# Optimization experiments

Measured on AMD Instinct MI355X. Metric: run time of the kernel, lower is better.

Reference implementation:

```python
import jax, jax.numpy as jnp
import numpy as np

D = 2048
HQ = 32
HKV = 8
DH = D // HQ          # 64
GROUP = HQ // HKV     # 4
B, T = 2, 2048


def setup_inputs() -> dict:
    key = jax.random.key(0)
    ks = jax.random.split(key, 5)
    s = 0.02
    return {
        "x": jax.random.normal(ks[0], (B, T, D), dtype=jnp.float32),
        "Wq": jax.random.normal(ks[1], (D, D), dtype=jnp.float32) * s,
        "Wk": jax.random.normal(ks[2], (D, HKV * DH), dtype=jnp.float32) * s,
        "Wv": jax.random.normal(ks[3], (D, HKV * DH), dtype=jnp.float32) * s,
        "Wo": jax.random.normal(ks[4], (D, D), dtype=jnp.float32) * s,
    }


def reference(x, Wq, Wk, Wv, Wo):
    Bsz, Tlen, _ = x.shape
    # projections
    q = (x @ Wq).reshape(Bsz, Tlen, HQ, DH).transpose(0, 2, 1, 3)    # [B,hq,T,dh]
    k = (x @ Wk).reshape(Bsz, Tlen, HKV, DH).transpose(0, 2, 1, 3)   # [B,hkv,T,dh]
    v = (x @ Wv).reshape(Bsz, Tlen, HKV, DH).transpose(0, 2, 1, 3)
    # GQA: repeat each kv head GROUP times along the head dim
    k = jnp.repeat(k, GROUP, axis=1)                                  # [B,hq,T,dh]
    v = jnp.repeat(v, GROUP, axis=1)
    scale = 1.0 / jnp.sqrt(jnp.asarray(DH, dtype=x.dtype))
    att = jnp.einsum("bhqd,bhkd->bhqk", q, k) * scale                # [B,hq,T,T]
    p = jax.nn.softmax(att, axis=-1)
    out = jnp.einsum("bhqk,bhkd->bhqd", p, v)                        # [B,hq,T,dh]
    out = out.transpose(0, 2, 1, 3).reshape(Bsz, Tlen, D)            # [B,T,D]
    return out @ Wo
```

## Files before the change

kernel.cpp:

```cpp
#include <hip/hip_runtime.h>
#include <stdint.h>

typedef __bf16 bf16;
typedef __bf16 bf16x8 __attribute__((ext_vector_type(8)));
typedef __bf16 bf16x4_t __attribute__((ext_vector_type(4)));
typedef __bf16 bf16x2_t __attribute__((ext_vector_type(2)));
typedef float f32x4 __attribute__((ext_vector_type(4)));
typedef float f32x16 __attribute__((ext_vector_type(16)));
typedef unsigned int u32x4 __attribute__((ext_vector_type(4)));

#define HQ_N 32
#define DH_N 64
#define SEQ 2048
#define NTOK 4096

#if __has_builtin(__builtin_amdgcn_exp2f)
#define EXP2(x) __builtin_amdgcn_exp2f(x)
#else
#define EXP2(x) __expf((x) * 0.69314718056f)
#endif

#define QSCALE 0.18033688011112042f

__device__ __forceinline__ void async_ld16(const bf16* g, bf16* l) {
    __builtin_amdgcn_global_load_lds(
        (__attribute__((address_space(1))) void*)(uintptr_t)(g),
        (__attribute__((address_space(3))) void*)(uint32_t)(uintptr_t)(l),
        16, 0, 0);
}

__device__ __forceinline__ void perm32swap(unsigned &x, unsigned &y) {
#if __has_builtin(__builtin_amdgcn_permlane32_swap)
    auto r = __builtin_amdgcn_permlane32_swap((int)x, (int)y, false, false);
    x = (unsigned)r[0]; y = (unsigned)r[1];
#else
    asm("v_permlane32_swap_b32 %0, %1" : "+v"(x), "+v"(y));
#endif
}

__global__ __launch_bounds__(256) void k_prep(
    const float* __restrict__ x,
    const float* __restrict__ Wq, const float* __restrict__ Wk,
    const float* __restrict__ Wv, const float* __restrict__ Wo,
    bf16* __restrict__ xb, bf16* __restrict__ WqkvT, bf16* __restrict__ WoT)
{
    const int z = blockIdx.z;
    const int tid = threadIdx.x;

    if (z >= 4) {
        int i = ((z - 4) * 1024 + blockIdx.y * 32 + blockIdx.x) * 256 + tid;
        float4 f = ((const float4*)x)[i];
        bf16x4_t v = {(bf16)f.x, (bf16)f.y, (bf16)f.z, (bf16)f.w};
        ((bf16x4_t*)xb)[i] = v;
        return;
    }

    const float* in; bf16* out; int C;
    const int R = 2048;
    if      (z == 0) { in = Wq; out = WqkvT;                        C = 2048; }
    else if (z == 1) { in = Wk; out = WqkvT + (size_t)2048 * 2048;  C = 512;  }
    else if (z == 2) { in = Wv; out = WqkvT + (size_t)2560 * 2048;  C = 512;  }
    else             { in = Wo; out = WoT;                          C = 2048; }
    if (blockIdx.x * 64 >= C) return;

    __shared__ float t[64][65];
    const int c0 = blockIdx.x * 64, r0 = blockIdx.y * 64;
#pragma unroll
    for (int c = 0; c < 4; ++c) {
        int i = tid + c * 256;
        int row = i >> 4, cc = (i & 15) * 4;
        float4 v = *(const float4*)(in + (size_t)(r0 + row) * C + c0 + cc);
        t[row][cc + 0] = v.x; t[row][cc + 1] = v.y;
        t[row][cc + 2] = v.z; t[row][cc + 3] = v.w;
    }
    __syncthreads();
#pragma unroll
    for (int c = 0; c < 4; ++c) {
        int i = tid + c * 256;
        int row = i >> 4, cc = (i & 15) * 4;
        bf16x4_t v = {(bf16)t[cc + 0][row], (bf16)t[cc + 1][row],
                      (bf16)t[cc + 2][row], (bf16)t[cc + 3][row]};
        *(bf16x4_t*)(out + (size_t)(c0 + row) * R + r0 + cc) = v;
    }
}

__global__ __launch_bounds__(256, 3) void k_gemm(
    const bf16* __restrict__ A, const bf16* __restrict__ BT,
    int lda, int ldb, int M, int N, int K, int mode,
    float* __restrict__ Cf, int ldc,
    bf16* __restrict__ Qb, bf16* __restrict__ Kb, bf16* __restrict__ VTb)
{
    __shared__ bf16 S[16384];
    bf16* As = S;
    bf16* Bs = S + 8192;

    const int tid  = threadIdx.x;
    const int lane = tid & 63;
    const int w    = tid >> 6;
    const int l15  = lane & 15, quad = lane >> 4;
    const int l7   = l15 & 7;
    const int wm = (w >> 1) * 64, wn = (w & 1) * 64;

    const int mb = M >> 7;
    const int band = blockIdx.x / (mb * 8);
    const int rsr  = blockIdx.x % (mb * 8);
    const int mi = rsr >> 3, ni = band * 8 + (rsr & 7);

    const int srow = tid >> 3;
    const int sc8e = ((tid & 7) ^ (srow & 7)) * 8;
    const bf16* aP = A  + (size_t)(mi * 128 + srow) * lda + sc8e;
    const bf16* bP = BT + (size_t)(ni * 128 + srow) * ldb + sc8e;

    f32x4 acc[4][4] = {};

    for (int k0 = 0; k0 < K; k0 += 64) {
        __syncthreads();
#pragma unroll
        for (int c = 0; c < 4; ++c) {
            async_ld16(aP + (size_t)c * 32 * lda, &As[(tid + c * 256) * 8]);
            async_ld16(bP + (size_t)c * 32 * ldb, &Bs[(tid + c * 256) * 8]);
        }
        aP += 64; bP += 64;
        __syncthreads();
#pragma unroll
        for (int ks = 0; ks < 2; ++ks) {
            const int ch = 8 * (((ks << 2) | quad) ^ l7);
            bf16x8 af[4], bfr[4];
#pragma unroll
            for (int mt = 0; mt < 4; ++mt)
                af[mt] = *(const bf16x8*)(As + (wm + mt * 16 + l15) * 64 + ch);
#pragma unroll
            for (int nt = 0; nt < 4; ++nt)
                bfr[nt] = *(const bf16x8*)(Bs + (wn + nt * 16 + l15) * 64 + ch);
#pragma unroll
            for (int mt = 0; mt < 4; ++mt)
#pragma unroll
                for (int nt = 0; nt < 4; ++nt)
                    acc[mt][nt] = __builtin_amdgcn_mfma_f32_16x16x32_bf16(
                        af[mt], bfr[nt], acc[mt][nt], 0, 0, 0);
        }
    }

    if (mode == 2) {
#pragma unroll
        for (int mt = 0; mt < 4; ++mt)
#pragma unroll
            for (int nt = 0; nt < 4; ++nt) {
                int rg0 = mi * 128 + wm + mt * 16 + quad * 4;
                int cg  = ni * 128 + wn + nt * 16 + l15;
#pragma unroll
                for (int r = 0; r < 4; ++r)
                    Cf[(size_t)(rg0 + r) * ldc + cg] = acc[mt][nt][r];
            }
    } else if (ni < 16) {
#pragma unroll
        for (int mt = 0; mt < 4; ++mt)
#pragma unroll
            for (int nt = 0; nt < 4; ++nt) {
                int rg0 = mi * 128 + wm + mt * 16 + quad * 4;
                int cg  = ni * 128 + wn + nt * 16 + l15;
#pragma unroll
                for (int r = 0; r < 4; ++r)
                    Qb[(size_t)(rg0 + r) * 2048 + cg] = (bf16)(acc[mt][nt][r] * QSCALE);
            }
    } else if (ni < 20) {
#pragma unroll
        for (int mt = 0; mt < 4; ++mt)
#pragma unroll
            for (int nt = 0; nt < 4; ++nt) {
                int rg0 = mi * 128 + wm + mt * 16 + quad * 4;
                int cg  = ni * 128 + wn + nt * 16 + l15 - 2048;
#pragma unroll
                for (int r = 0; r < 4; ++r)
                    Kb[(size_t)(rg0 + r) * 512 + cg] = (bf16)acc[mt][nt][r];
            }
    } else {
        __syncthreads();
#pragma unroll
        for (int mt = 0; mt < 4; ++mt)
#pragma unroll
            for (int nt = 0; nt < 4; ++nt) {
                int rl0 = wm + mt * 16 + quad * 4;
                int cl  = wn + nt * 16 + l15;
#pragma unroll
                for (int r = 0; r < 4; ++r)
                    S[cl * 128 + rl0 + r] = (bf16)acc[mt][nt][r];
            }
        __syncthreads();
        const int v0 = ni * 128 - 2560;
#pragma unroll
        for (int c = 0; c < 8; ++c) {
            int i = tid + c * 256;
            int row = i >> 4, c8 = (i & 15) * 8;
            uint4 vv = *(const uint4*)(S + row * 128 + c8);
            *(uint4*)(VTb + (size_t)(v0 + row) * NTOK + mi * 128 + c8) = vv;
        }
    }
}

__global__ __launch_bounds__(128, 2) void k_attn(
    const bf16* __restrict__ Qb,
    const bf16* __restrict__ Kb,
    const bf16* __restrict__ VTb,
    bf16* __restrict__ Ob)
{
    __shared__ bf16 Ks[64 * 64];
    __shared__ bf16 Vt[64 * 64];

    const int tid  = threadIdx.x;
    const int lane = tid & 63;
    const int w    = tid >> 6;
    const int c31  = lane & 31;
    const int half = lane >> 5;
    const int r7   = c31 & 7;

    const int bid = (blockIdx.x & 7) * 128 + (blockIdx.x >> 3);
    const int qt  = bid & 15;
    const int hq  = (bid >> 4) & 31;
    const int b   = bid >> 9;
    const int hkv = hq >> 2;
    const int q0  = qt * 128 + w * 64;
    const size_t tokbase = (size_t)b * SEQ;

    const int srow = tid >> 3;
    const int sc8e = ((tid & 7) ^ (srow & 7)) * 8;
    const bf16* kP = Kb  + (tokbase + srow) * 512 + hkv * DH_N + sc8e;
    const bf16* vP = VTb + ((size_t)hkv * DH_N + srow) * NTOK + tokbase + sc8e;

    bf16x8 qf[2][4];
#pragma unroll
    for (int qb = 0; qb < 2; ++qb)
#pragma unroll
        for (int ks = 0; ks < 4; ++ks)
            qf[qb][ks] = *(const bf16x8*)(
                Qb + (tokbase + q0 + qb * 32 + c31) * 2048 + hq * DH_N + ks * 16 + half * 8);

    f32x16 acc_o[2][2] = {};
    float lsum[2] = {0.f, 0.f};

    for (int kt = 0; kt < 32; ++kt) {
        const int k0 = kt * 64;
        __syncthreads();
#pragma unroll
        for (int c = 0; c < 4; ++c) {
            async_ld16(kP + (size_t)(k0 + c * 16) * 512, &Ks[(tid + c * 128) * 8]);
            async_ld16(vP + (size_t)c * 16 * NTOK + k0,  &Vt[(tid + c * 128) * 8]);
        }
        __syncthreads();

        f32x16 accs[2][2] = {};
#pragma unroll
        for (int ks = 0; ks < 4; ++ks)
#pragma unroll
            for (int mb = 0; mb < 2; ++mb) {
                bf16x8 kf = *(const bf16x8*)(
                    Ks + (mb * 32 + c31) * 64 + (((ks << 1) | half) ^ r7) * 8);
                accs[mb][0] = __builtin_amdgcn_mfma_f32_32x32x16_bf16(
                    kf, qf[0][ks], accs[mb][0], 0, 0, 0);
                accs[mb][1] = __builtin_amdgcn_mfma_f32_32x32x16_bf16(
                    kf, qf[1][ks], accs[mb][1], 0, 0, 0);
            }

        unsigned pk[2][2][8];
#pragma unroll
        for (int mb = 0; mb < 2; ++mb)
#pragma unroll
            for (int qb = 0; qb < 2; ++qb)
#pragma unroll
                for (int g = 0; g < 4; ++g) {
                    float p0 = EXP2(accs[mb][qb][4 * g + 0]);
                    float p1 = EXP2(accs[mb][qb][4 * g + 1]);
                    float p2 = EXP2(accs[mb][qb][4 * g + 2]);
                    float p3 = EXP2(accs[mb][qb][4 * g + 3]);
                    lsum[qb] += (p0 + p1) + (p2 + p3);
                    bf16x2_t w0 = {(bf16)p0, (bf16)p1};
                    bf16x2_t w1 = {(bf16)p2, (bf16)p3};
                    pk[mb][qb][g * 2 + 0] = __builtin_bit_cast(unsigned, w0);
                    pk[mb][qb][g * 2 + 1] = __builtin_bit_cast(unsigned, w1);
                }

#pragma unroll
        for (int ks = 0; ks < 4; ++ks) {
            const int mb = ks >> 1, par = ks & 1;
            bf16x8 pf[2];
#pragma unroll
            for (int qb = 0; qb < 2; ++qb) {
                unsigned x0 = pk[mb][qb][(2 * par + 0) * 2 + 0];
                unsigned y0 = pk[mb][qb][(2 * par + 1) * 2 + 0];
                unsigned x1 = pk[mb][qb][(2 * par + 0) * 2 + 1];
                unsigned y1 = pk[mb][qb][(2 * par + 1) * 2 + 1];
                perm32swap(x0, y0);
                perm32swap(x1, y1);
                u32x4 fr = {x0, x1, y0, y1};
                pf[qb] = __builtin_bit_cast(bf16x8, fr);
            }
#pragma unroll
            for (int db = 0; db < 2; ++db) {
                bf16x8 vf = *(const bf16x8*)(
                    Vt + (db * 32 + c31) * 64 + (((ks << 1) | half) ^ r7) * 8);
                acc_o[db][0] = __builtin_amdgcn_mfma_f32_32x32x16_bf16(
                    vf, pf[0], acc_o[db][0], 0, 0, 0);
                acc_o[db][1] = __builtin_amdgcn_mfma_f32_32x32x16_bf16(
                    vf, pf[1], acc_o[db][1], 0, 0, 0);
            }
        }
    }

    __syncthreads();

    float rl[2];
#pragma unroll
    for (int qb = 0; qb < 2; ++qb) {
        float s = lsum[qb];
        s += __shfl_xor(s, 32);
        rl[qb] = 1.0f / s;
    }

    bf16* W = w ? Vt : Ks;
#pragma unroll
    for (int db = 0; db < 2; ++db)
#pragma unroll
        for (int qb = 0; qb < 2; ++qb) {
            const int q = qb * 32 + c31;
#pragma unroll
            for (int g = 0; g < 4; ++g) {
                bf16x4_t o4 = {(bf16)(acc_o[db][qb][4 * g + 0] * rl[qb]),
                               (bf16)(acc_o[db][qb][4 * g + 1] * rl[qb]),
                               (bf16)(acc_o[db][qb][4 * g + 2] * rl[qb]),
                               (bf16)(acc_o[db][qb][4 * g + 3] * rl[qb])};
                const int ch = db * 4 + g;
                *(bf16x4_t*)&W[q * 64 + ((ch ^ (q & 7)) * 8) + half * 4] = o4;
            }
        }
#pragma unroll
    for (int cc = 0; cc < 8; ++cc) {
        int qr = (lane >> 3) + cc * 8;
        int ci = lane & 7;
        bf16x8 ov = *(const bf16x8*)&W[qr * 64 + ((ci ^ (qr & 7)) * 8)];
        *(bf16x8*)(Ob + (tokbase + q0 + qr) * 2048 + hq * DH_N + ci * 8) = ov;
    }
}

extern "C" void kernel_launch(void* const* d_in, const int* in_sizes, int n_in,
                              void* d_out, int out_size, void* d_ws, size_t ws_size,
                              hipStream_t stream)
{
    const float* x  = (const float*)d_in[0];
    const float* Wq = (const float*)d_in[1];
    const float* Wk = (const float*)d_in[2];
    const float* Wv = (const float*)d_in[3];
    const float* Wo = (const float*)d_in[4];
    float* out = (float*)d_out;

    bf16* ws    = (bf16*)d_ws;
    bf16* xb    = ws;
    bf16* WqkvT = xb    + (size_t)4096 * 2048;
    bf16* WoT   = WqkvT + (size_t)3072 * 2048;
    bf16* Qb    = WoT   + (size_t)2048 * 2048;
    bf16* Kb    = Qb    + (size_t)4096 * 2048;
    bf16* VTb   = Kb    + (size_t)4096 * 512;
    bf16* Ob    = VTb   + (size_t)512 * 4096;

    k_prep<<<dim3(32, 32, 12), 256, 0, stream>>>(
        x, Wq, Wk, Wv, Wo, xb, WqkvT, WoT);

    k_gemm<<<(4096 / 128) * (3072 / 128), 256, 0, stream>>>(
        xb, WqkvT, 2048, 2048, 4096, 3072, 2048, 1,
        nullptr, 0, Qb, Kb, VTb);

    k_attn<<<1024, 128, 0, stream>>>(Qb, Kb, VTb, Ob);

    k_gemm<<<(4096 / 128) * (2048 / 128), 256, 0, stream>>>(
        Ob, WoT, 2048, 2048, 4096, 2048, 2048, 2,
        out, 2048, nullptr, nullptr, nullptr);
}
```

Baseline: 286.1 us.

## Split attention KV range across two wave pairs and reduce partial outputs in LDS

The attention block grows from 2 to 4 waves. Each pair of waves handles half of the key sequence with its own K/V shared-memory tiles, and the partial outputs and row sums are then merged through LDS before normalization and store. The aim is more parallelism per query tile, shorter serial key loops and better latency hiding. It also restructures the score MFMA loop per mb block to cut live accumulator registers. The costs are extra LDS, a reduction phase with additional barriers, and a larger block that may limit occupancy.

```diff
diff --git a/kernel.cpp b/kernel.cpp
--- a/kernel.cpp
+++ b/kernel.cpp
@@ -198,18 +198,20 @@
     }
 }
 
-__global__ __launch_bounds__(128, 2) void k_attn(
+__global__ __launch_bounds__(256, 3) void k_attn(
     const bf16* __restrict__ Qb,
     const bf16* __restrict__ Kb,
     const bf16* __restrict__ VTb,
     bf16* __restrict__ Ob)
 {
-    __shared__ bf16 Ks[64 * 64];
-    __shared__ bf16 Vt[64 * 64];
+    __shared__ bf16 KV[16384];
+    __shared__ float Lred[2][2][64];
 
     const int tid  = threadIdx.x;
     const int lane = tid & 63;
     const int w    = tid >> 6;
+    const int qw   = w & 1;
+    const int kw   = w >> 1;
     const int c31  = lane & 31;
     const int half = lane >> 5;
     const int r7   = c31 & 7;
@@ -219,11 +221,15 @@
     const int hq  = (bid >> 4) & 31;
     const int b   = bid >> 9;
     const int hkv = hq >> 2;
-    const int q0  = qt * 128 + w * 64;
+    const int q0  = qt * 128 + qw * 64;
     const size_t tokbase = (size_t)b * SEQ;
 
-    const int srow = tid >> 3;
-    const int sc8e = ((tid & 7) ^ (srow & 7)) * 8;
+    bf16* Ksw = KV + kw * 8192;
+    bf16* Vtw = Ksw + 4096;
+
+    const int gtid = tid & 127;
+    const int srow = gtid >> 3;
+    const int sc8e = ((gtid & 7) ^ (srow & 7)) * 8;
     const bf16* kP = Kb  + (tokbase + srow) * 512 + hkv * DH_N + sc8e;
     const bf16* vP = VTb + ((size_t)hkv * DH_N + srow) * NTOK + tokbase + sc8e;
 
@@ -238,46 +244,44 @@
     f32x16 acc_o[2][2] = {};
     float lsum[2] = {0.f, 0.f};
 
-    for (int kt = 0; kt < 32; ++kt) {
-        const int k0 = kt * 64;
+    for (int kt = 0; kt < 16; ++kt) {
+        const int k0 = (kw * 16 + kt) * 64;
         __syncthreads();
 #pragma unroll
         for (int c = 0; c < 4; ++c) {
-            async_ld16(kP + (size_t)(k0 + c * 16) * 512, &Ks[(tid + c * 128) * 8]);
-            async_ld16(vP + (size_t)c * 16 * NTOK + k0,  &Vt[(tid + c * 128) * 8]);
-        }
-        __syncthreads();
-
-        f32x16 accs[2][2] = {};
-#pragma unroll
-        for (int ks = 0; ks < 4; ++ks)
-#pragma unroll
-            for (int mb = 0; mb < 2; ++mb) {
+            async_ld16(kP + (size_t)(k0 + c * 16) * 512, &Ksw[(gtid + c * 128) * 8]);
+            async_ld16(vP + (size_t)c * 16 * NTOK + k0,  &Vtw[(gtid + c * 128) * 8]);
+        }
+        __syncthreads();
+
+        unsigned pk[2][2][8];
+#pragma unroll
+        for (int mb = 0; mb < 2; ++mb) {
+            f32x16 sa[2] = {};
+#pragma unroll
+            for (int ks = 0; ks < 4; ++ks) {
                 bf16x8 kf = *(const bf16x8*)(
-                    Ks + (mb * 32 + c31) * 64 + (((ks << 1) | half) ^ r7) * 8);
-                accs[mb][0] = __builtin_amdgcn_mfma_f32_32x32x16_bf16(
-                    kf, qf[0][ks], accs[mb][0], 0, 0, 0);
-                accs[mb][1] = __builtin_amdgcn_mfma_f32_32x32x16_bf16(
-                    kf, qf[1][ks], accs[mb][1], 0, 0, 0);
-            }
-
-        unsigned pk[2][2][8];
-#pragma unroll
-        for (int mb = 0; mb < 2; ++mb)
+                    Ksw + (mb * 32 + c31) * 64 + (((ks << 1) | half) ^ r7) * 8);
+                sa[0] = __builtin_amdgcn_mfma_f32_32x32x16_bf16(
+                    kf, qf[0][ks], sa[0], 0, 0, 0);
+                sa[1] = __builtin_amdgcn_mfma_f32_32x32x16_bf16(
+                    kf, qf[1][ks], sa[1], 0, 0, 0);
+            }
 #pragma unroll
             for (int qb = 0; qb < 2; ++qb)
 #pragma unroll
                 for (int g = 0; g < 4; ++g) {
-                    float p0 = EXP2(accs[mb][qb][4 * g + 0]);
-                    float p1 = EXP2(accs[mb][qb][4 * g + 1]);
-                    float p2 = EXP2(accs[mb][qb][4 * g + 2]);
-                    float p3 = EXP2(accs[mb][qb][4 * g + 3]);
+                    float p0 = EXP2(sa[qb][4 * g + 0]);
+                    float p1 = EXP2(sa[qb][4 * g + 1]);
+                    float p2 = EXP2(sa[qb][4 * g + 2]);
+                    float p3 = EXP2(sa[qb][4 * g + 3]);
                     lsum[qb] += (p0 + p1) + (p2 + p3);
                     bf16x2_t w0 = {(bf16)p0, (bf16)p1};
                     bf16x2_t w1 = {(bf16)p2, (bf16)p3};
                     pk[mb][qb][g * 2 + 0] = __builtin_bit_cast(unsigned, w0);
                     pk[mb][qb][g * 2 + 1] = __builtin_bit_cast(unsigned, w1);
                 }
+        }
 
 #pragma unroll
         for (int ks = 0; ks < 4; ++ks) {
@@ -297,7 +301,7 @@
 #pragma unroll
             for (int db = 0; db < 2; ++db) {
                 bf16x8 vf = *(const bf16x8*)(
-                    Vt + (db * 32 + c31) * 64 + (((ks << 1) | half) ^ r7) * 8);
+                    Vtw + (db * 32 + c31) * 64 + (((ks << 1) | half) ^ r7) * 8);
                 acc_o[db][0] = __builtin_amdgcn_mfma_f32_32x32x16_bf16(
                     vf, pf[0], acc_o[db][0], 0, 0, 0);
                 acc_o[db][1] = __builtin_amdgcn_mfma_f32_32x32x16_bf16(
@@ -307,37 +311,66 @@
     }
 
     __syncthreads();
-
-    float rl[2];
-#pragma unroll
-    for (int qb = 0; qb < 2; ++qb) {
-        float s = lsum[qb];
-        s += __shfl_xor(s, 32);
-        rl[qb] = 1.0f / s;
-    }
-
-    bf16* W = w ? Vt : Ks;
-#pragma unroll
-    for (int db = 0; db < 2; ++db)
+    float* Red = (float*)KV;
+    if (kw == 1) {
+#pragma unroll
+        for (int db = 0; db < 2; ++db)
+#pragma unroll
+            for (int qb = 0; qb < 2; ++qb)
+#pragma unroll
+                for (int r = 0; r < 16; ++r)
+                    Red[qw * 4096 + ((db * 2 + qb) * 16 + r) * 64 + lane] =
+                        acc_o[db][qb][r];
+        Lred[qw][0][lane] = lsum[0];
+        Lred[qw][1][lane] = lsum[1];
+    }
+    __syncthreads();
+    if (kw == 0) {
+#pragma unroll
+        for (int db = 0; db < 2; ++db)
+#pragma unroll
+            for (int qb = 0; qb < 2; ++qb)
+#pragma unroll
+                for (int r = 0; r < 16; ++r)
+                    acc_o[db][qb][r] +=
+                        Red[qw * 4096 + ((db * 2 + qb) * 16 + r) * 64 + lane];
+        lsum[0] += Lred[qw][0][lane];
+        lsum[1] += Lred[qw][1][lane];
+    }
+    __syncthreads();
+
+    if (kw == 0) {
+        float rl[2];
 #pragma unroll
         for (int qb = 0; qb < 2; ++qb) {
-            const int q = qb * 32 + c31;
-#pragma unroll
-            for (int g = 0; g < 4; ++g) {
-                bf16x4_t o4 = {(bf16)(acc_o[db][qb][4 * g + 0] * rl[qb]),
-                               (bf16)(acc_o[db][qb][4 * g + 1] * rl[qb]),
-                               (bf16)(acc_o[db][qb][4 * g + 2] * rl[qb]),
-                               (bf16)(acc_o[db][qb][4 * g + 3] * rl[qb])};
-                const int ch = db * 4 + g;
-                *(bf16x4_t*)&W[q * 64 + ((ch ^ (q & 7)) * 8) + half * 4] = o4;
-            }
-        }
-#pragma unroll
-    for (int cc = 0; cc < 8; ++cc) {
-        int qr = (lane >> 3) + cc * 8;
-        int ci = lane & 7;
-        bf16x8 ov = *(const bf16x8*)&W[qr * 64 + ((ci ^ (qr & 7)) * 8)];
-        *(bf16x8*)(Ob + (tokbase + q0 + qr) * 2048 + hq * DH_N + ci * 8) = ov;
+            float s = lsum[qb];
+            s += __shfl_xor(s, 32);
+            rl[qb] = 1.0f / s;
+        }
+
+        bf16* W = (bf16*)KV + qw * 4096;
+#pragma unroll
+        for (int db = 0; db < 2; ++db)
+#pragma unroll
+            for (int qb = 0; qb < 2; ++qb) {
+                const int q = qb * 32 + c31;
+#pragma unroll
+                for (int g = 0; g < 4; ++g) {
+                    bf16x4_t o4 = {(bf16)(acc_o[db][qb][4 * g + 0] * rl[qb]),
+                                   (bf16)(acc_o[db][qb][4 * g + 1] * rl[qb]),
+                                   (bf16)(acc_o[db][qb][4 * g + 2] * rl[qb]),
+                                   (bf16)(acc_o[db][qb][4 * g + 3] * rl[qb])};
+                    const int ch = db * 4 + g;
+                    *(bf16x4_t*)&W[q * 64 + ((ch ^ (q & 7)) * 8) + half * 4] = o4;
+                }
+            }
+#pragma unroll
+        for (int cc = 0; cc < 8; ++cc) {
+            int qr = (lane >> 3) + cc * 8;
+            int ci = lane & 7;
+            bf16x8 ov = *(const bf16x8*)&W[qr * 64 + ((ci ^ (qr & 7)) * 8)];
+            *(bf16x8*)(Ob + (tokbase + q0 + qr) * 2048 + hq * DH_N + ci * 8) = ov;
+        }
     }
 }
 
@@ -368,7 +401,7 @@
         xb, WqkvT, 2048, 2048, 4096, 3072, 2048, 1,
         nullptr, 0, Qb, Kb, VTb);
 
-    k_attn<<<1024, 128, 0, stream>>>(Qb, Kb, VTb, Ob);
+    k_attn<<<1024, 256, 0, stream>>>(Qb, Kb, VTb, Ob);
 
     k_gemm<<<(4096 / 128) * (2048 / 128), 256, 0, stream>>>(
         Ob, WoT, 2048, 2048, 4096, 2048, 2048, 2,
```

Result: slower. 376.5 us (+31.6%).

## Double-buffer K/V tiles in attention kernel and raise MFMA wave priority

Applied to the files above, without the earlier changes.

Attention K and V tiles now go into two LDS buffers. The next tile's async global-to-LDS loads are issued before the current tile is computed, so load latency overlaps with the MFMA work. The two barriers per iteration become one waitcnt plus barrier at the end, and s_setprio brackets the MFMA sections. LDS use doubles to 32KB per block, which may limit occupancy at 2 blocks per CU.

```diff
diff --git a/kernel.cpp b/kernel.cpp
--- a/kernel.cpp
+++ b/kernel.cpp
@@ -204,8 +204,7 @@
     const bf16* __restrict__ VTb,
     bf16* __restrict__ Ob)
 {
-    __shared__ bf16 Ks[64 * 64];
-    __shared__ bf16 Vt[64 * 64];
+    __shared__ bf16 KV[2][8192];
 
     const int tid  = threadIdx.x;
     const int lane = tid & 63;
@@ -238,28 +237,42 @@
     f32x16 acc_o[2][2] = {};
     float lsum[2] = {0.f, 0.f};
 
+    auto STAGE = [&](int kt, int buf) {
+        bf16* Kd = &KV[buf][0];
+        bf16* Vd = &KV[buf][4096];
+        const int k0 = kt * 64;
+#pragma unroll
+        for (int c = 0; c < 4; ++c) {
+            async_ld16(kP + (size_t)(k0 + c * 16) * 512, &Kd[(tid + c * 128) * 8]);
+            async_ld16(vP + (size_t)c * 16 * NTOK + k0,  &Vd[(tid + c * 128) * 8]);
+        }
+    };
+
+    STAGE(0, 0);
+    asm volatile("s_waitcnt vmcnt(0)" ::: "memory");
+    __builtin_amdgcn_s_barrier();
+
+    int cur = 0;
     for (int kt = 0; kt < 32; ++kt) {
-        const int k0 = kt * 64;
-        __syncthreads();
-#pragma unroll
-        for (int c = 0; c < 4; ++c) {
-            async_ld16(kP + (size_t)(k0 + c * 16) * 512, &Ks[(tid + c * 128) * 8]);
-            async_ld16(vP + (size_t)c * 16 * NTOK + k0,  &Vt[(tid + c * 128) * 8]);
-        }
-        __syncthreads();
+        if (kt < 31) STAGE(kt + 1, cur ^ 1);
+
+        const bf16* Ksw = &KV[cur][0];
+        const bf16* Vtw = &KV[cur][4096];
 
         f32x16 accs[2][2] = {};
+        __builtin_amdgcn_s_setprio(1);
 #pragma unroll
         for (int ks = 0; ks < 4; ++ks)
 #pragma unroll
             for (int mb = 0; mb < 2; ++mb) {
                 bf16x8 kf = *(const bf16x8*)(
-                    Ks + (mb * 32 + c31) * 64 + (((ks << 1) | half) ^ r7) * 8);
+                    Ksw + (mb * 32 + c31) * 64 + (((ks << 1) | half) ^ r7) * 8);
                 accs[mb][0] = __builtin_amdgcn_mfma_f32_32x32x16_bf16(
                     kf, qf[0][ks], accs[mb][0], 0, 0, 0);
                 accs[mb][1] = __builtin_amdgcn_mfma_f32_32x32x16_bf16(
                     kf, qf[1][ks], accs[mb][1], 0, 0, 0);
             }
+        __builtin_amdgcn_s_setprio(0);
 
         unsigned pk[2][2][8];
 #pragma unroll
@@ -294,19 +307,23 @@
                 u32x4 fr = {x0, x1, y0, y1};
                 pf[qb] = __builtin_bit_cast(bf16x8, fr);
             }
+            __builtin_amdgcn_s_setprio(1);
 #pragma unroll
             for (int db = 0; db < 2; ++db) {
                 bf16x8 vf = *(const bf16x8*)(
-                    Vt + (db * 32 + c31) * 64 + (((ks << 1) | half) ^ r7) * 8);
+                    Vtw + (db * 32 + c31) * 64 + (((ks << 1) | half) ^ r7) * 8);
                 acc_o[db][0] = __builtin_amdgcn_mfma_f32_32x32x16_bf16(
                     vf, pf[0], acc_o[db][0], 0, 0, 0);
                 acc_o[db][1] = __builtin_amdgcn_mfma_f32_32x32x16_bf16(
                     vf, pf[1], acc_o[db][1], 0, 0, 0);
             }
-        }
-    }
-
-    __syncthreads();
+            __builtin_amdgcn_s_setprio(0);
+        }
+
+        asm volatile("s_waitcnt vmcnt(0)" ::: "memory");
+        __builtin_amdgcn_s_barrier();
+        cur ^= 1;
+    }
 
     float rl[2];
 #pragma unroll
@@ -316,7 +333,7 @@
         rl[qb] = 1.0f / s;
     }
 
-    bf16* W = w ? Vt : Ks;
+    bf16* W = &KV[0][0] + w * 4096;
 #pragma unroll
     for (int db = 0; db < 2; ++db)
 #pragma unroll
```

Measured after the change: 292.8 us. +2.4%, slower.

## Replace GEMM with 256x256-tile, 8-wave, double-buffered pipelined kernel

Applied to the files above, without the earlier changes.

Replaces the 128x128 single-buffered GEMM with a 256x256 tile kernel using 512 threads (8 waves). It double-buffers LDS in half-tile quarters and interleaves async global-to-LDS loads with MFMA phases, using explicit barriers, vmcnt waits and setprio. It also remaps blocks with an XCD-aware swizzle and adapts the Q/K/V epilogues to the larger tile. The aim is to hide load latency and raise data reuse, at the cost of far fewer blocks (192 and 128) and possible load imbalance across CUs.

```diff
diff --git a/kernel.cpp b/kernel.cpp
--- a/kernel.cpp
+++ b/kernel.cpp
@@ -37,6 +37,10 @@
     asm("v_permlane32_swap_b32 %0, %1" : "+v"(x), "+v"(y));
 #endif
 }
+
+#define GBAR()  do { __builtin_amdgcn_s_barrier(); __builtin_amdgcn_sched_barrier(0); } while (0)
+#define VMW4()  do { asm volatile("s_waitcnt vmcnt(4)" ::: "memory"); __builtin_amdgcn_sched_barrier(0); } while (0)
+#define VMW0()  do { asm volatile("s_waitcnt vmcnt(0)" ::: "memory"); __builtin_amdgcn_sched_barrier(0); } while (0)
 
 __global__ __launch_bounds__(256) void k_prep(
     const float* __restrict__ x,
@@ -84,116 +88,167 @@
     }
 }
 
-__global__ __launch_bounds__(256, 3) void k_gemm(
+__global__ __launch_bounds__(512, 2) void k_gemm8(
     const bf16* __restrict__ A, const bf16* __restrict__ BT,
     int lda, int ldb, int M, int N, int K, int mode,
     float* __restrict__ Cf, int ldc,
     bf16* __restrict__ Qb, bf16* __restrict__ Kb, bf16* __restrict__ VTb)
 {
-    __shared__ bf16 S[16384];
-    bf16* As = S;
-    bf16* Bs = S + 8192;
+    __shared__ bf16 S[2][4][8192];
 
     const int tid  = threadIdx.x;
     const int lane = tid & 63;
     const int w    = tid >> 6;
-    const int l15  = lane & 15, quad = lane >> 4;
-    const int l7   = l15 & 7;
-    const int wm = (w >> 1) * 64, wn = (w & 1) * 64;
-
-    const int mb = M >> 7;
-    const int band = blockIdx.x / (mb * 8);
-    const int rsr  = blockIdx.x % (mb * 8);
-    const int mi = rsr >> 3, ni = band * 8 + (rsr & 7);
-
-    const int srow = tid >> 3;
-    const int sc8e = ((tid & 7) ^ (srow & 7)) * 8;
-    const bf16* aP = A  + (size_t)(mi * 128 + srow) * lda + sc8e;
-    const bf16* bP = BT + (size_t)(ni * 128 + srow) * ldb + sc8e;
-
-    f32x4 acc[4][4] = {};
-
-    for (int k0 = 0; k0 < K; k0 += 64) {
-        __syncthreads();
-#pragma unroll
-        for (int c = 0; c < 4; ++c) {
-            async_ld16(aP + (size_t)c * 32 * lda, &As[(tid + c * 256) * 8]);
-            async_ld16(bP + (size_t)c * 32 * ldb, &Bs[(tid + c * 256) * 8]);
-        }
-        aP += 64; bP += 64;
-        __syncthreads();
-#pragma unroll
-        for (int ks = 0; ks < 2; ++ks) {
-            const int ch = 8 * (((ks << 2) | quad) ^ l7);
-            bf16x8 af[4], bfr[4];
+    const int l15  = lane & 15, quad = lane >> 4, l7 = l15 & 7;
+    const int wm   = (w >> 2) * 64;
+    const int wn   = (w & 3) * 32;
+
+    const int cpx = gridDim.x >> 3;
+    const int swz = (blockIdx.x & 7) * cpx + (blockIdx.x >> 3);
+    const int mi = swz & 15, ni = swz >> 4;
+
+    const int rr = tid >> 3;
+    const int sc = ((tid & 7) ^ (rr & 7)) * 8;
+    const bf16* aP = A  + (size_t)(mi * 256 + rr) * lda + sc;
+    const bf16* bP = BT + (size_t)(ni * 256 + rr) * ldb + sc;
+    const int nt = K >> 6;
+
+    f32x4 acc[2][2][4][2] = {};
+
+    auto SA = [&](int t, int h, int buf) {
+        bf16* d = &S[buf][h][tid * 8];
+        const bf16* s = aP + (size_t)(h * 128) * lda + t * 64;
+        async_ld16(s, d);
+        async_ld16(s + (size_t)64 * lda, d + 4096);
+    };
+    auto SB_ = [&](int t, int h, int buf) {
+        bf16* d = &S[buf][2 + h][tid * 8];
+        const bf16* s = bP + (size_t)(h * 128) * ldb + t * 64;
+        async_ld16(s, d);
+        async_ld16(s + (size_t)64 * ldb, d + 4096);
+    };
+    auto LA = [&](bf16x8 af[4][2], int buf, int mh) {
+#pragma unroll
+        for (int mt = 0; mt < 4; ++mt)
+#pragma unroll
+            for (int ks = 0; ks < 2; ++ks)
+                af[mt][ks] = *(const bf16x8*)&S[buf][mh][
+                    (wm + mt * 16 + l15) * 64 + (((ks << 2) | quad) ^ l7) * 8];
+    };
+    auto LB = [&](bf16x8 bf_[2][2], int buf, int nh) {
+#pragma unroll
+        for (int nt2 = 0; nt2 < 2; ++nt2)
+#pragma unroll
+            for (int ks = 0; ks < 2; ++ks)
+                bf_[nt2][ks] = *(const bf16x8*)&S[buf][2 + nh][
+                    (wn + nt2 * 16 + l15) * 64 + (((ks << 2) | quad) ^ l7) * 8];
+    };
+    auto MMA = [&](int mh, int nh, bf16x8 af[4][2], bf16x8 bf_[2][2]) {
+        __builtin_amdgcn_s_setprio(1);
+#pragma unroll
+        for (int ks = 0; ks < 2; ++ks)
 #pragma unroll
             for (int mt = 0; mt < 4; ++mt)
-                af[mt] = *(const bf16x8*)(As + (wm + mt * 16 + l15) * 64 + ch);
-#pragma unroll
-            for (int nt = 0; nt < 4; ++nt)
-                bfr[nt] = *(const bf16x8*)(Bs + (wn + nt * 16 + l15) * 64 + ch);
-#pragma unroll
-            for (int mt = 0; mt < 4; ++mt)
-#pragma unroll
-                for (int nt = 0; nt < 4; ++nt)
-                    acc[mt][nt] = __builtin_amdgcn_mfma_f32_16x16x32_bf16(
-                        af[mt], bfr[nt], acc[mt][nt], 0, 0, 0);
-        }
-    }
+#pragma unroll
+                for (int nt2 = 0; nt2 < 2; ++nt2)
+                    acc[mh][nh][mt][nt2] = __builtin_amdgcn_mfma_f32_16x16x32_bf16(
+                        af[mt][ks], bf_[nt2][ks], acc[mh][nh][mt][nt2], 0, 0, 0);
+        __builtin_amdgcn_s_setprio(0);
+    };
+
+    auto TILE = [&](int t, int buf) {
+        bf16x8 af[4][2], bflo[2][2], bfhi[2][2];
+        LA(af, buf, 0); LB(bflo, buf, 0);
+        if (t + 1 < nt) SB_(t + 1, 0, buf ^ 1);
+        GBAR(); MMA(0, 0, af, bflo); GBAR();
+        LB(bfhi, buf, 1);
+        if (t + 1 < nt) SA(t + 1, 1, buf ^ 1);
+        GBAR(); MMA(0, 1, af, bfhi); GBAR();
+        LA(af, buf, 1);
+        if (t + 2 < nt) SA(t + 2, 0, buf);
+        GBAR(); MMA(1, 1, af, bfhi); GBAR();
+        if (t + 2 < nt) SB_(t + 2, 1, buf);
+        GBAR(); MMA(1, 0, af, bflo);
+        if (t < nt - 3) { VMW4(); } else { VMW0(); }
+        GBAR();
+    };
+
+    SA(0, 0, 0); SB_(0, 0, 0); SB_(0, 1, 0); SA(0, 1, 0);
+    SA(1, 0, 1); SB_(1, 1, 1);
+    VMW4(); GBAR();
+
+    for (int t2 = 0; t2 < nt; t2 += 2) { TILE(t2, 0); TILE(t2 + 1, 1); }
 
     if (mode == 2) {
 #pragma unroll
+        for (int mh = 0; mh < 2; ++mh)
+#pragma unroll
+        for (int nh = 0; nh < 2; ++nh)
+#pragma unroll
         for (int mt = 0; mt < 4; ++mt)
 #pragma unroll
-            for (int nt = 0; nt < 4; ++nt) {
-                int rg0 = mi * 128 + wm + mt * 16 + quad * 4;
-                int cg  = ni * 128 + wn + nt * 16 + l15;
-#pragma unroll
-                for (int r = 0; r < 4; ++r)
-                    Cf[(size_t)(rg0 + r) * ldc + cg] = acc[mt][nt][r];
-            }
-    } else if (ni < 16) {
+        for (int nt2 = 0; nt2 < 2; ++nt2) {
+            int rg0 = mi * 256 + mh * 128 + wm + mt * 16 + quad * 4;
+            int cg  = ni * 256 + nh * 128 + wn + nt2 * 16 + l15;
+#pragma unroll
+            for (int r = 0; r < 4; ++r)
+                Cf[(size_t)(rg0 + r) * ldc + cg] = acc[mh][nh][mt][nt2][r];
+        }
+    } else if (ni < 8) {
+#pragma unroll
+        for (int mh = 0; mh < 2; ++mh)
+#pragma unroll
+        for (int nh = 0; nh < 2; ++nh)
 #pragma unroll
         for (int mt = 0; mt < 4; ++mt)
 #pragma unroll
-            for (int nt = 0; nt < 4; ++nt) {
-                int rg0 = mi * 128 + wm + mt * 16 + quad * 4;
-                int cg  = ni * 128 + wn + nt * 16 + l15;
-#pragma unroll
-                for (int r = 0; r < 4; ++r)
-                    Qb[(size_t)(rg0 + r) * 2048 + cg] = (bf16)(acc[mt][nt][r] * QSCALE);
-            }
-    } else if (ni < 20) {
+        for (int nt2 = 0; nt2 < 2; ++nt2) {
+            int rg0 = mi * 256 + mh * 128 + wm + mt * 16 + quad * 4;
+            int cg  = ni * 256 + nh * 128 + wn + nt2 * 16 + l15;
+#pragma unroll
+            for (int r = 0; r < 4; ++r)
+                Qb[(size_t)(rg0 + r) * 2048 + cg] = (bf16)(acc[mh][nh][mt][nt2][r] * QSCALE);
+        }
+    } else if (ni < 10) {
+#pragma unroll
+        for (int mh = 0; mh < 2; ++mh)
+#pragma unroll
+        for (int nh = 0; nh < 2; ++nh)
 #pragma unroll
         for (int mt = 0; mt < 4; ++mt)
 #pragma unroll
-            for (int nt = 0; nt < 4; ++nt) {
-                int rg0 = mi * 128 + wm + mt * 16 + quad * 4;
-                int cg  = ni * 128 + wn + nt * 16 + l15 - 2048;
-#pragma unroll
-                for (int r = 0; r < 4; ++r)
-                    Kb[(size_t)(rg0 + r) * 512 + cg] = (bf16)acc[mt][nt][r];
-            }
+        for (int nt2 = 0; nt2 < 2; ++nt2) {
+            int rg0 = mi * 256 + mh * 128 + wm + mt * 16 + quad * 4;
+            int cg  = ni * 256 + nh * 128 + wn + nt2 * 16 + l15 - 2048;
+#pragma unroll
+            for (int r = 0; r < 4; ++r)
+                Kb[(size_t)(rg0 + r) * 512 + cg] = (bf16)acc[mh][nh][mt][nt2][r];
+        }
     } else {
         __syncthreads();
+        bf16* SBp = (bf16*)S;
+#pragma unroll
+        for (int mh = 0; mh < 2; ++mh)
+#pragma unroll
+        for (int nh = 0; nh < 2; ++nh)
 #pragma unroll
         for (int mt = 0; mt < 4; ++mt)
 #pragma unroll
-            for (int nt = 0; nt < 4; ++nt) {
-                int rl0 = wm + mt * 16 + quad * 4;
-                int cl  = wn + nt * 16 + l15;
-#pragma unroll
-                for (int r = 0; r < 4; ++r)
-                    S[cl * 128 + rl0 + r] = (bf16)acc[mt][nt][r];
-            }
+        for (int nt2 = 0; nt2 < 2; ++nt2) {
+            int rl0 = mh * 128 + wm + mt * 16 + quad * 4;
+            int cl  = nh * 128 + wn + nt2 * 16 + l15;
+#pragma unroll
+            for (int r = 0; r < 4; ++r)
+                SBp[cl * 256 + rl0 + r] = (bf16)acc[mh][nh][mt][nt2][r];
+        }
         __syncthreads();
-        const int v0 = ni * 128 - 2560;
-#pragma unroll
-        for (int c = 0; c < 8; ++c) {
-            int i = tid + c * 256;
-            int row = i >> 4, c8 = (i & 15) * 8;
-            uint4 vv = *(const uint4*)(S + row * 128 + c8);
-            *(uint4*)(VTb + (size_t)(v0 + row) * NTOK + mi * 128 + c8) = vv;
+        const int v0 = ni * 256 - 2560;
+#pragma unroll
+        for (int it = 0; it < 16; ++it) {
+            int cl = (tid >> 5) + it * 16;
+            int tk = (tid & 31) * 8;
+            uint4 vv = *(const uint4*)(SBp + cl * 256 + tk);
+            *(uint4*)(VTb + (size_t)(v0 + cl) * NTOK + mi * 256 + tk) = vv;
         }
     }
 }
@@ -364,13 +419,13 @@
     k_prep<<<dim3(32, 32, 12), 256, 0, stream>>>(
         x, Wq, Wk, Wv, Wo, xb, WqkvT, WoT);
 
-    k_gemm<<<(4096 / 128) * (3072 / 128), 256, 0, stream>>>(
+    k_gemm8<<<192, 512, 0, stream>>>(
         xb, WqkvT, 2048, 2048, 4096, 3072, 2048, 1,
         nullptr, 0, Qb, Kb, VTb);
 
     k_attn<<<1024, 128, 0, stream>>>(Qb, Kb, VTb, Ob);
 
-    k_gemm<<<(4096 / 128) * (2048 / 128), 256, 0, stream>>>(
+    k_gemm8<<<128, 512, 0, stream>>>(
         Ob, WoT, 2048, 2048, 4096, 2048, 2048, 2,
         out, 2048, nullptr, nullptr, nullptr);
 }
```

After: 307.1 us. 7.4% more time.
